# Kernel optimization log

Hardware: AMD Instinct MI355X
Metric: run time of the kernel (lower is better)

## Reference

```python
import jax, jax.numpy as jnp
import numpy as np

B, S, D, T = 512, 65536, 256, 10   # graphs, substructures, emb_dim, num_tasks
THRESHOLD = 0.4                    # CausalGNN threshold default
MEMBER_P = 0.002                   # ~131 substructures per graph


def setup_inputs() -> dict:
    key = jax.random.key(0)
    ks = jax.random.split(key, 8)
    def w(k, shape):
        fan_in = shape[0]
        return jax.random.normal(k, shape, jnp.float32) / np.float32(np.sqrt(fan_in))
    return {
        "h_graph": jax.random.normal(ks[0], (B, D), jnp.float32),
        "h_sub":   jax.random.normal(ks[1], (S, D), jnp.float32),
        "W1": w(ks[2], (D, 2 * D)),  "b1": jnp.zeros((2 * D,), jnp.float32),
        "W2": w(ks[3], (2 * D, 1)),  "b2": jnp.zeros((1,), jnp.float32),
        "Wc": w(ks[4], (2 * D, T)),  "bc": jnp.zeros((T,), jnp.float32),
        # dense [B,S] bool membership: mask[i,j] = substructure j belongs to graph i
        "mask": jax.random.bernoulli(ks[5], MEMBER_P, (B, S)),
    }


def _l2_normalize(x, eps=1e-12):  # F.normalize(p=2, dim=1)
    n = jnp.linalg.norm(x, axis=1, keepdims=True)
    return x / jnp.maximum(n, eps)


def reference(h_graph, h_sub, W1, b1, W2, b2, Wc, bc, mask):
    # SubMaskGenerator: Linear -> ReLU -> Dropout(eval=identity) -> Linear -> sigmoid, squeeze
    gate_logits = (jax.nn.relu(h_sub @ W1 + b1) @ W2 + b2)[:, 0]      # [S]
    subgraph_mask = jax.nn.sigmoid(gate_logits)                        # [S]

    # fused masked segment mean (replaces per-graph python loop + host sync):
    # valid[i,j] = (sub j in graph i) & (gate > threshold)
    valid = mask & (subgraph_mask > THRESHOLD)                         # [B,S] bool
    w = valid.astype(h_sub.dtype)
    counts = w.sum(axis=1, keepdims=True)                              # [B,1]
    sums = w @ h_sub                                                   # [B,D]
    h_sub_aligned = jnp.where(counts > 0, sums / jnp.maximum(counts, 1.0), 0.0)

    h_sub_norm = _l2_normalize(h_sub_aligned)
    h_graph_norm = _l2_normalize(h_graph)
    # F.cosine_similarity(dim=1, eps=1e-8) on the already-normalized vectors
    na = jnp.linalg.norm(h_sub_norm, axis=1)
    ng = jnp.linalg.norm(h_graph_norm, axis=1)
    cos = (h_sub_norm * h_graph_norm).sum(axis=1) / (
        jnp.maximum(na, 1e-8) * jnp.maximum(ng, 1e-8))
    cosine_loss = 1.0 - cos.mean()

    h_combined = jnp.concatenate([h_graph, h_sub_aligned], axis=1)     # [B,2D]
    logits = h_combined @ Wc + bc                                      # [B,T]
    return logits, cosine_loss, subgraph_mask
```

## Files before the change

kernel.cpp:

```cpp
#include <hip/hip_runtime.h>
#include <math.h>

#define D 256
#define H 512
#define TT 10
#define THRESH 0.4f
#define KS 8
#define NSPLIT 16

typedef __attribute__((ext_vector_type(8))) _Float16 half8;
typedef __attribute__((ext_vector_type(4))) float f32x4;

__global__ __launch_bounds__(256) void w1_prep(const float* __restrict__ W1,
                                               short* __restrict__ W1s)
{
    const int tid = blockIdx.x * 256 + threadIdx.x;
    const int lane = tid & 63;
    const int cell = tid >> 6;
    const int k = cell & 7;
    const int n = cell >> 3;
    const int row0 = k * 32 + (lane >> 4) * 8;
    const int col = n * 16 + (lane & 15);
    _Float16 h8[8];
    #pragma unroll
    for (int i = 0; i < 8; ++i)
        h8[i] = (_Float16)W1[(size_t)(row0 + i) * H + col];
    *reinterpret_cast<half8*>(W1s + (((size_t)n * 8 + k) * 64 + lane) * 8) =
        *reinterpret_cast<half8*>(h8);
}

__global__ __launch_bounds__(256, 2) void gate_mfma(
    const float* __restrict__ h_sub,
    const short* __restrict__ W1s,
    const float* __restrict__ b1,
    const float* __restrict__ W2,
    const float* __restrict__ b2,
    float* __restrict__ submask,
    unsigned* __restrict__ gbits)
{
    __shared__ __align__(16) short sB[2][16384];
    __shared__ float sb1[H], sw2[H];
    const int tid = threadIdx.x;
    const int lane = tid & 63;
    const int w = tid >> 6;
    const int base = blockIdx.x * 128 + w * 32;
    const int rot = blockIdx.x & 7;
    const float bb = b2[0];

    {
        int i = tid * 2;
        *reinterpret_cast<float2*>(&sb1[i]) = *reinterpret_cast<const float2*>(&b1[i]);
        *reinterpret_cast<float2*>(&sw2[i]) = *reinterpret_cast<const float2*>(&W2[i]);
    }

    half8 af[2][KS];
    #pragma unroll
    for (int s = 0; s < 2; ++s) {
        const int row = base + s * 16 + (lane & 15);
        const float* rp = h_sub + (size_t)row * D + (lane >> 4) * 8;
        #pragma unroll
        for (int k = 0; k < KS; ++k) {
            float x[8];
            *reinterpret_cast<float4*>(&x[0]) =
                *reinterpret_cast<const float4*>(rp + k * 32);
            *reinterpret_cast<float4*>(&x[4]) =
                *reinterpret_cast<const float4*>(rp + k * 32 + 4);
            _Float16 h8[8];
            #pragma unroll
            for (int i = 0; i < 8; ++i) h8[i] = (_Float16)x[i];
            af[s][k] = *reinterpret_cast<half8*>(h8);
        }
    }

    __syncthreads();

    auto stage = [&](int cc, int b) {
        const int c = (cc + rot) & 7;
        const char* gp = (const char*)W1s + ((size_t)c << 15) + (size_t)tid * 16;
        char* lp0 = (char*)&sB[b][0] + (size_t)tid * 16;
        #pragma unroll
        for (int i = 0; i < 8; ++i) {
            __builtin_amdgcn_global_load_lds(
                (const __attribute__((address_space(1))) void*)(gp + i * 4096),
                (__attribute__((address_space(3))) void*)(lp0 + i * 4096),
                16, 0, 0);
        }
    };

    stage(0, 0);
    stage(1, 1);

    float lp[2][4] = {{0.f,0.f,0.f,0.f},{0.f,0.f,0.f,0.f}};

    for (int cc = 0; cc < 8; ++cc) {
        if (cc < 7) asm volatile("s_waitcnt vmcnt(8)" ::: "memory");
        else        asm volatile("s_waitcnt vmcnt(0)" ::: "memory");
        __builtin_amdgcn_s_barrier();
        __builtin_amdgcn_sched_barrier(0);

        const short* buf = &sB[cc & 1][0];
        const int c = (cc + rot) & 7;

        f32x4 acc[2][4];
        #pragma unroll
        for (int s = 0; s < 2; ++s)
            #pragma unroll
            for (int nt = 0; nt < 4; ++nt)
                acc[s][nt] = (f32x4){0.f,0.f,0.f,0.f};

        __builtin_amdgcn_s_setprio(1);
        #pragma unroll
        for (int k = 0; k < KS; ++k) {
            half8 bh0 = *reinterpret_cast<const half8*>(buf + ((0 * 8 + k) * 64 + lane) * 8);
            half8 bh1 = *reinterpret_cast<const half8*>(buf + ((1 * 8 + k) * 64 + lane) * 8);
            half8 bh2 = *reinterpret_cast<const half8*>(buf + ((2 * 8 + k) * 64 + lane) * 8);
            half8 bh3 = *reinterpret_cast<const half8*>(buf + ((3 * 8 + k) * 64 + lane) * 8);
            acc[0][0] = __builtin_amdgcn_mfma_f32_16x16x32_f16(af[0][k], bh0, acc[0][0], 0, 0, 0);
            acc[1][0] = __builtin_amdgcn_mfma_f32_16x16x32_f16(af[1][k], bh0, acc[1][0], 0, 0, 0);
            acc[0][1] = __builtin_amdgcn_mfma_f32_16x16x32_f16(af[0][k], bh1, acc[0][1], 0, 0, 0);
            acc[1][1] = __builtin_amdgcn_mfma_f32_16x16x32_f16(af[1][k], bh1, acc[1][1], 0, 0, 0);
            acc[0][2] = __builtin_amdgcn_mfma_f32_16x16x32_f16(af[0][k], bh2, acc[0][2], 0, 0, 0);
            acc[1][2] = __builtin_amdgcn_mfma_f32_16x16x32_f16(af[1][k], bh2, acc[1][2], 0, 0, 0);
            acc[0][3] = __builtin_amdgcn_mfma_f32_16x16x32_f16(af[0][k], bh3, acc[0][3], 0, 0, 0);
            acc[1][3] = __builtin_amdgcn_mfma_f32_16x16x32_f16(af[1][k], bh3, acc[1][3], 0, 0, 0);
        }
        __builtin_amdgcn_s_setprio(0);

        #pragma unroll
        for (int nt = 0; nt < 4; ++nt) {
            const int hc = c * 64 + nt * 16 + (lane & 15);
            const float b1h = sb1[hc], w2h = sw2[hc];
            #pragma unroll
            for (int s = 0; s < 2; ++s)
                #pragma unroll
                for (int j = 0; j < 4; ++j) {
                    float v = acc[s][nt][j] + b1h;
                    v = v > 0.f ? v : 0.f;
                    lp[s][j] = fmaf(v, w2h, lp[s][j]);
                }
        }

        __builtin_amdgcn_sched_barrier(0);
        __builtin_amdgcn_s_barrier();
        if (cc < 6) stage(cc + 2, cc & 1);
    }

    #pragma unroll
    for (int m = 1; m < 16; m <<= 1)
        #pragma unroll
        for (int s = 0; s < 2; ++s)
            #pragma unroll
            for (int j = 0; j < 4; ++j)
                lp[s][j] += __shfl_xor(lp[s][j], m);

    const int g = lane >> 4;
    unsigned bits = 0;
    float sig[2][4];
    #pragma unroll
    for (int s = 0; s < 2; ++s)
        #pragma unroll
        for (int j = 0; j < 4; ++j) {
            sig[s][j] = 1.f / (1.f + expf(-(lp[s][j] + bb)));
            if (sig[s][j] > THRESH) bits |= 1u << (s * 16 + g * 4 + j);
        }
    bits |= __shfl_xor(bits, 16);
    bits |= __shfl_xor(bits, 32);
    if (lane == 0) gbits[blockIdx.x * 4 + w] = bits;

    if ((lane & 15) == 0)
        #pragma unroll
        for (int s = 0; s < 2; ++s)
            #pragma unroll
            for (int j = 0; j < 4; ++j)
                submask[base + s * 16 + g * 4 + j] = sig[s][j];
}

__global__ __launch_bounds__(256) void seg_scan(
    const float* __restrict__ h_sub,
    const int*   __restrict__ mask,
    const unsigned* __restrict__ gbits,
    float* __restrict__ psum,
    int*   __restrict__ pcnt,
    int S)
{
    const int i = blockIdx.x / NSPLIT;
    const int p = blockIdx.x % NSPLIT;
    const int tid = threadIdx.x;
    const int lane = tid & 63;
    const int w = tid >> 6;
    const int seg = S / NSPLIT;
    const int start = p * seg;
    const int* mrow = mask + (size_t)i * S + start;

    __shared__ unsigned sbits[4096 / 32];
    if (tid < seg / 32) sbits[tid] = gbits[(start >> 5) + tid];

    const int wbase = w * 1024;
    int4 m4[4];
    #pragma unroll
    for (int it = 0; it < 4; ++it)
        m4[it] = *reinterpret_cast<const int4*>(mrow + wbase + it * 256 + (lane << 2));

    __syncthreads();

    float4 acc = make_float4(0.f, 0.f, 0.f, 0.f);
    int cnt = 0;

    #pragma unroll
    for (int it = 0; it < 4; ++it) {
        const int j0 = wbase + it * 256 + (lane << 2);
        const unsigned bw = sbits[j0 >> 5];
        const int sh = j0 & 31;
        unsigned long long bal[4];
        bal[0] = __ballot((m4[it].x != 0) & ((bw >> (sh + 0)) & 1u));
        bal[1] = __ballot((m4[it].y != 0) & ((bw >> (sh + 1)) & 1u));
        bal[2] = __ballot((m4[it].z != 0) & ((bw >> (sh + 2)) & 1u));
        bal[3] = __ballot((m4[it].w != 0) & ((bw >> (sh + 3)) & 1u));
        #pragma unroll
        for (int s = 0; s < 4; ++s) {
            unsigned long long b = bal[s];
            while (b) {
                int t = __builtin_ctzll(b);
                b &= b - 1;
                int jj = start + wbase + it * 256 + (t << 2) + s;
                float4 hv = *reinterpret_cast<const float4*>(
                    h_sub + (size_t)jj * D + (lane << 2));
                acc.x += hv.x; acc.y += hv.y; acc.z += hv.z; acc.w += hv.w;
                cnt++;
            }
        }
    }

    __shared__ float ssum[4][D];
    __shared__ int   scnt[4];
    *reinterpret_cast<float4*>(&ssum[w][lane << 2]) = acc;
    if (lane == 0) scnt[w] = cnt;
    __syncthreads();

    float a = ssum[0][tid] + ssum[1][tid] + ssum[2][tid] + ssum[3][tid];
    psum[(size_t)blockIdx.x * D + tid] = a;
    if (tid == 0) pcnt[blockIdx.x] = scnt[0] + scnt[1] + scnt[2] + scnt[3];
}

__global__ __launch_bounds__(256) void seg_combine(
    const float* __restrict__ h_graph,
    const float* __restrict__ psum,
    const int*   __restrict__ pcnt,
    const float* __restrict__ Wc,
    const float* __restrict__ bc,
    float* __restrict__ logits,
    float* __restrict__ cos_ws)
{
    const int i = blockIdx.x;
    const int tid = threadIdx.x;
    const int lane = tid & 63;
    const int w = tid >> 6;

    float a = 0.f;
    int c = 0;
    #pragma unroll
    for (int p = 0; p < NSPLIT; ++p) {
        a += psum[((size_t)i * NSPLIT + p) * D + tid];
        c += pcnt[i * NSPLIT + p];
    }
    a = (c > 0) ? (a / (float)c) : 0.f;
    const float g = h_graph[(size_t)i * D + tid];

    float r0 = a * a, r1 = g * g, r2 = a * g;
    #pragma unroll
    for (int m = 1; m < 64; m <<= 1) {
        r0 += __shfl_xor(r0, m);
        r1 += __shfl_xor(r1, m);
        r2 += __shfl_xor(r2, m);
    }
    __shared__ float red[4][3];
    if (lane == 0) { red[w][0] = r0; red[w][1] = r1; red[w][2] = r2; }
    __syncthreads();
    if (tid == 0) {
        float a2 = red[0][0] + red[1][0] + red[2][0] + red[3][0];
        float g2 = red[0][1] + red[1][1] + red[2][1] + red[3][1];
        float ag = red[0][2] + red[1][2] + red[2][2] + red[3][2];
        float an = sqrtf(a2), gn = sqrtf(g2);
        float cs = (c > 0) ? (ag / (fmaxf(an, 1e-12f) * fmaxf(gn, 1e-12f))) : 0.f;
        cos_ws[i] = cs;
    }

    float lg[TT];
    #pragma unroll
    for (int t = 0; t < TT; ++t)
        lg[t] = g * Wc[(size_t)tid * TT + t] + a * Wc[(size_t)(D + tid) * TT + t];
    #pragma unroll
    for (int m = 1; m < 64; m <<= 1)
        #pragma unroll
        for (int t = 0; t < TT; ++t) lg[t] += __shfl_xor(lg[t], m);
    __shared__ float lpart[4][TT];
    if (lane == 0)
        #pragma unroll
        for (int t = 0; t < TT; ++t) lpart[w][t] = lg[t];
    __syncthreads();
    if (tid < TT)
        logits[(size_t)i * TT + tid] =
            lpart[0][tid] + lpart[1][tid] + lpart[2][tid] + lpart[3][tid] + bc[tid];
}

__global__ void loss_kernel(const float* __restrict__ cos_ws,
                            float* __restrict__ out, int B)
{
    const int lane = threadIdx.x;
    float s = 0.f;
    for (int i = lane; i < B; i += 64) s += cos_ws[i];
    #pragma unroll
    for (int m = 1; m < 64; m <<= 1) s += __shfl_xor(s, m);
    if (lane == 0) out[0] = 1.0f - s / (float)B;
}

extern "C" void kernel_launch(void* const* d_in, const int* in_sizes, int n_in,
                              void* d_out, int out_size, void* d_ws, size_t ws_size,
                              hipStream_t stream)
{
    const float* h_graph = (const float*)d_in[0];
    const float* h_sub   = (const float*)d_in[1];
    const float* W1      = (const float*)d_in[2];
    const float* b1      = (const float*)d_in[3];
    const float* W2      = (const float*)d_in[4];
    const float* b2      = (const float*)d_in[5];
    const float* Wc      = (const float*)d_in[6];
    const float* bc      = (const float*)d_in[7];
    const int*   mask    = (const int*)d_in[8];

    const int B = in_sizes[0] / D;
    const int S = in_sizes[1] / D;

    float* out     = (float*)d_out;
    float* logits  = out;
    float* loss    = out + (size_t)B * TT;
    float* submask = loss + 1;

    char* ws = (char*)d_ws;
    short*    W1s    = (short*)ws;
    unsigned* gbits  = (unsigned*)(ws + 512 * 1024);
    int*      pcnt   = (int*)(ws + 528 * 1024);
    float*    cos_ws = (float*)(ws + 576 * 1024);
    float*    psum   = (float*)(ws + 1024 * 1024);

    w1_prep<<<64, 256, 0, stream>>>(W1, W1s);
    gate_mfma<<<S / 128, 256, 0, stream>>>(h_sub, W1s, b1, W2, b2, submask, gbits);
    seg_scan<<<B * NSPLIT, 256, 0, stream>>>(h_sub, mask, gbits, psum, pcnt, S);
    seg_combine<<<B, 256, 0, stream>>>(h_graph, psum, pcnt, Wc, bc, logits, cos_ws);
    loss_kernel<<<1, 64, 0, stream>>>(cos_ws, loss, B);
}
```

Baseline: 71.66 us.

## Compress membership mask into bitmasks inside gate kernel with extra waves

The gate kernel grows to 512 threads: four waves keep doing the MFMA gate MLP while four new waves read the dense int32 membership mask and pack it into 64-bit ballot bitmasks in workspace. The seg_scan kernel then reads these compact bitmasks instead of the 128 MB int mask. The aim is to overlap the memory-bound mask read with the compute-bound gate work and shrink what seg_scan has to load. In exchange, the larger block may lower occupancy for the gate waves, and the mask waves have to join the gate waves' barriers.

```diff
diff --git a/kernel.cpp b/kernel.cpp
--- a/kernel.cpp
+++ b/kernel.cpp
@@ -29,50 +29,26 @@
         *reinterpret_cast<half8*>(h8);
 }
 
-__global__ __launch_bounds__(256, 2) void gate_mfma(
+__global__ __launch_bounds__(512, 4) void gate_fused(
     const float* __restrict__ h_sub,
     const short* __restrict__ W1s,
     const float* __restrict__ b1,
     const float* __restrict__ W2,
     const float* __restrict__ b2,
+    const int*   __restrict__ mask,
     float* __restrict__ submask,
-    unsigned* __restrict__ gbits)
+    unsigned* __restrict__ gbits,
+    unsigned long long* __restrict__ cmask)
 {
     __shared__ __align__(16) short sB[2][16384];
     __shared__ float sb1[H], sw2[H];
     const int tid = threadIdx.x;
     const int lane = tid & 63;
     const int w = tid >> 6;
+    const bool isGate = (w < 4);
     const int base = blockIdx.x * 128 + w * 32;
     const int rot = blockIdx.x & 7;
     const float bb = b2[0];
-
-    {
-        int i = tid * 2;
-        *reinterpret_cast<float2*>(&sb1[i]) = *reinterpret_cast<const float2*>(&b1[i]);
-        *reinterpret_cast<float2*>(&sw2[i]) = *reinterpret_cast<const float2*>(&W2[i]);
-    }
-
-    half8 af[2][KS];
-    #pragma unroll
-    for (int s = 0; s < 2; ++s) {
-        const int row = base + s * 16 + (lane & 15);
-        const float* rp = h_sub + (size_t)row * D + (lane >> 4) * 8;
-        #pragma unroll
-        for (int k = 0; k < KS; ++k) {
-            float x[8];
-            *reinterpret_cast<float4*>(&x[0]) =
-                *reinterpret_cast<const float4*>(rp + k * 32);
-            *reinterpret_cast<float4*>(&x[4]) =
-                *reinterpret_cast<const float4*>(rp + k * 32 + 4);
-            _Float16 h8[8];
-            #pragma unroll
-            for (int i = 0; i < 8; ++i) h8[i] = (_Float16)x[i];
-            af[s][k] = *reinterpret_cast<half8*>(h8);
-        }
-    }
-
-    __syncthreads();
 
     auto stage = [&](int cc, int b) {
         const int c = (cc + rot) & 7;
@@ -87,97 +63,152 @@
         }
     };
 
-    stage(0, 0);
-    stage(1, 1);
+    half8 af[2][KS];
+
+    if (isGate) {
+        stage(0, 0);
+        stage(1, 1);
+        int i = tid * 2;
+        *reinterpret_cast<float2*>(&sb1[i]) = *reinterpret_cast<const float2*>(&b1[i]);
+        *reinterpret_cast<float2*>(&sw2[i]) = *reinterpret_cast<const float2*>(&W2[i]);
+
+        #pragma unroll
+        for (int s = 0; s < 2; ++s) {
+            const int row = base + s * 16 + (lane & 15);
+            const float* rp = h_sub + (size_t)row * D + (lane >> 4) * 8;
+            #pragma unroll
+            for (int k = 0; k < KS; ++k) {
+                float x[8];
+                *reinterpret_cast<float4*>(&x[0]) =
+                    *reinterpret_cast<const float4*>(rp + k * 32);
+                *reinterpret_cast<float4*>(&x[4]) =
+                    *reinterpret_cast<const float4*>(rp + k * 32 + 4);
+                _Float16 h8[8];
+                #pragma unroll
+                for (int i2 = 0; i2 < 8; ++i2) h8[i2] = (_Float16)x[i2];
+                af[s][k] = *reinterpret_cast<half8*>(h8);
+            }
+        }
+    }
+
+    __syncthreads();
 
     float lp[2][4] = {{0.f,0.f,0.f,0.f},{0.f,0.f,0.f,0.f}};
+    const int mw = blockIdx.x * 4 + (w - 4);
+    const size_t g0 = (size_t)mw * 64;
 
     for (int cc = 0; cc < 8; ++cc) {
-        if (cc < 7) asm volatile("s_waitcnt vmcnt(8)" ::: "memory");
-        else        asm volatile("s_waitcnt vmcnt(0)" ::: "memory");
-        __builtin_amdgcn_s_barrier();
-        __builtin_amdgcn_sched_barrier(0);
-
-        const short* buf = &sB[cc & 1][0];
-        const int c = (cc + rot) & 7;
-
-        f32x4 acc[2][4];
+        if (isGate) {
+            if (cc < 7) asm volatile("s_waitcnt vmcnt(8)" ::: "memory");
+            else        asm volatile("s_waitcnt vmcnt(0)" ::: "memory");
+            __builtin_amdgcn_s_barrier();
+            __builtin_amdgcn_sched_barrier(0);
+
+            const short* buf = &sB[cc & 1][0];
+            const int c = (cc + rot) & 7;
+
+            f32x4 acc[2][4];
+            #pragma unroll
+            for (int s = 0; s < 2; ++s)
+                #pragma unroll
+                for (int nt = 0; nt < 4; ++nt)
+                    acc[s][nt] = (f32x4){0.f,0.f,0.f,0.f};
+
+            __builtin_amdgcn_s_setprio(1);
+            #pragma unroll
+            for (int k = 0; k < KS; ++k) {
+                half8 bh0 = *reinterpret_cast<const half8*>(buf + ((0 * 8 + k) * 64 + lane) * 8);
+                half8 bh1 = *reinterpret_cast<const half8*>(buf + ((1 * 8 + k) * 64 + lane) * 8);
+                half8 bh2 = *reinterpret_cast<const half8*>(buf + ((2 * 8 + k) * 64 + lane) * 8);
+                half8 bh3 = *reinterpret_cast<const half8*>(buf + ((3 * 8 + k) * 64 + lane) * 8);
+                acc[0][0] = __builtin_amdgcn_mfma_f32_16x16x32_f16(af[0][k], bh0, acc[0][0], 0, 0, 0);
+                acc[1][0] = __builtin_amdgcn_mfma_f32_16x16x32_f16(af[1][k], bh0, acc[1][0], 0, 0, 0);
+                acc[0][1] = __builtin_amdgcn_mfma_f32_16x16x32_f16(af[0][k], bh1, acc[0][1], 0, 0, 0);
+                acc[1][1] = __builtin_amdgcn_mfma_f32_16x16x32_f16(af[1][k], bh1, acc[1][1], 0, 0, 0);
+                acc[0][2] = __builtin_amdgcn_mfma_f32_16x16x32_f16(af[0][k], bh2, acc[0][2], 0, 0, 0);
+                acc[1][2] = __builtin_amdgcn_mfma_f32_16x16x32_f16(af[1][k], bh2, acc[1][2], 0, 0, 0);
+                acc[0][3] = __builtin_amdgcn_mfma_f32_16x16x32_f16(af[0][k], bh3, acc[0][3], 0, 0, 0);
+                acc[1][3] = __builtin_amdgcn_mfma_f32_16x16x32_f16(af[1][k], bh3, acc[1][3], 0, 0, 0);
+            }
+            __builtin_amdgcn_s_setprio(0);
+
+            #pragma unroll
+            for (int nt = 0; nt < 4; ++nt) {
+                const int hc = c * 64 + nt * 16 + (lane & 15);
+                const float b1h = sb1[hc], w2h = sw2[hc];
+                #pragma unroll
+                for (int s = 0; s < 2; ++s)
+                    #pragma unroll
+                    for (int j = 0; j < 4; ++j) {
+                        float v = acc[s][nt][j] + b1h;
+                        v = v > 0.f ? v : 0.f;
+                        lp[s][j] = fmaf(v, w2h, lp[s][j]);
+                    }
+            }
+
+            __builtin_amdgcn_sched_barrier(0);
+            __builtin_amdgcn_s_barrier();
+            if (cc < 6) stage(cc + 2, cc & 1);
+        } else {
+            __builtin_amdgcn_s_barrier();
+            {
+                const size_t gbase = g0 + (size_t)cc * 8;
+                int4 m4[8];
+                #pragma unroll
+                for (int u = 0; u < 8; ++u)
+                    m4[u] = *reinterpret_cast<const int4*>(
+                        mask + (gbase + u) * 256 + (lane << 2));
+                #pragma unroll
+                for (int u = 0; u < 8; ++u) {
+                    unsigned long long c0 = __ballot(m4[u].x != 0);
+                    unsigned long long c1 = __ballot(m4[u].y != 0);
+                    unsigned long long c2 = __ballot(m4[u].z != 0);
+                    unsigned long long c3 = __ballot(m4[u].w != 0);
+                    if (lane == 0) {
+                        unsigned long long* cp = cmask + (gbase + u) * 4;
+                        cp[0] = c0; cp[1] = c1; cp[2] = c2; cp[3] = c3;
+                    }
+                }
+            }
+            __builtin_amdgcn_s_barrier();
+        }
+    }
+
+    if (isGate) {
+        #pragma unroll
+        for (int m = 1; m < 16; m <<= 1)
+            #pragma unroll
+            for (int s = 0; s < 2; ++s)
+                #pragma unroll
+                for (int j = 0; j < 4; ++j)
+                    lp[s][j] += __shfl_xor(lp[s][j], m);
+
+        const int g = lane >> 4;
+        unsigned bits = 0;
+        float sig[2][4];
         #pragma unroll
         for (int s = 0; s < 2; ++s)
             #pragma unroll
-            for (int nt = 0; nt < 4; ++nt)
-                acc[s][nt] = (f32x4){0.f,0.f,0.f,0.f};
-
-        __builtin_amdgcn_s_setprio(1);
-        #pragma unroll
-        for (int k = 0; k < KS; ++k) {
-            half8 bh0 = *reinterpret_cast<const half8*>(buf + ((0 * 8 + k) * 64 + lane) * 8);
-            half8 bh1 = *reinterpret_cast<const half8*>(buf + ((1 * 8 + k) * 64 + lane) * 8);
-            half8 bh2 = *reinterpret_cast<const half8*>(buf + ((2 * 8 + k) * 64 + lane) * 8);
-            half8 bh3 = *reinterpret_cast<const half8*>(buf + ((3 * 8 + k) * 64 + lane) * 8);
-            acc[0][0] = __builtin_amdgcn_mfma_f32_16x16x32_f16(af[0][k], bh0, acc[0][0], 0, 0, 0);
-            acc[1][0] = __builtin_amdgcn_mfma_f32_16x16x32_f16(af[1][k], bh0, acc[1][0], 0, 0, 0);
-            acc[0][1] = __builtin_amdgcn_mfma_f32_16x16x32_f16(af[0][k], bh1, acc[0][1], 0, 0, 0);
-            acc[1][1] = __builtin_amdgcn_mfma_f32_16x16x32_f16(af[1][k], bh1, acc[1][1], 0, 0, 0);
-            acc[0][2] = __builtin_amdgcn_mfma_f32_16x16x32_f16(af[0][k], bh2, acc[0][2], 0, 0, 0);
-            acc[1][2] = __builtin_amdgcn_mfma_f32_16x16x32_f16(af[1][k], bh2, acc[1][2], 0, 0, 0);
-            acc[0][3] = __builtin_amdgcn_mfma_f32_16x16x32_f16(af[0][k], bh3, acc[0][3], 0, 0, 0);
-            acc[1][3] = __builtin_amdgcn_mfma_f32_16x16x32_f16(af[1][k], bh3, acc[1][3], 0, 0, 0);
-        }
-        __builtin_amdgcn_s_setprio(0);
-
-        #pragma unroll
-        for (int nt = 0; nt < 4; ++nt) {
-            const int hc = c * 64 + nt * 16 + (lane & 15);
-            const float b1h = sb1[hc], w2h = sw2[hc];
+            for (int j = 0; j < 4; ++j) {
+                sig[s][j] = 1.f / (1.f + expf(-(lp[s][j] + bb)));
+                if (sig[s][j] > THRESH) bits |= 1u << (s * 16 + g * 4 + j);
+            }
+        bits |= __shfl_xor(bits, 16);
+        bits |= __shfl_xor(bits, 32);
+        if (lane == 0) gbits[blockIdx.x * 4 + w] = bits;
+
+        if ((lane & 15) == 0)
             #pragma unroll
             for (int s = 0; s < 2; ++s)
                 #pragma unroll
-                for (int j = 0; j < 4; ++j) {
-                    float v = acc[s][nt][j] + b1h;
-                    v = v > 0.f ? v : 0.f;
-                    lp[s][j] = fmaf(v, w2h, lp[s][j]);
-                }
-        }
-
-        __builtin_amdgcn_sched_barrier(0);
-        __builtin_amdgcn_s_barrier();
-        if (cc < 6) stage(cc + 2, cc & 1);
-    }
-
-    #pragma unroll
-    for (int m = 1; m < 16; m <<= 1)
-        #pragma unroll
-        for (int s = 0; s < 2; ++s)
-            #pragma unroll
-            for (int j = 0; j < 4; ++j)
-                lp[s][j] += __shfl_xor(lp[s][j], m);
-
-    const int g = lane >> 4;
-    unsigned bits = 0;
-    float sig[2][4];
-    #pragma unroll
-    for (int s = 0; s < 2; ++s)
-        #pragma unroll
-        for (int j = 0; j < 4; ++j) {
-            sig[s][j] = 1.f / (1.f + expf(-(lp[s][j] + bb)));
-            if (sig[s][j] > THRESH) bits |= 1u << (s * 16 + g * 4 + j);
-        }
-    bits |= __shfl_xor(bits, 16);
-    bits |= __shfl_xor(bits, 32);
-    if (lane == 0) gbits[blockIdx.x * 4 + w] = bits;
-
-    if ((lane & 15) == 0)
-        #pragma unroll
-        for (int s = 0; s < 2; ++s)
-            #pragma unroll
-            for (int j = 0; j < 4; ++j)
-                submask[base + s * 16 + g * 4 + j] = sig[s][j];
+                for (int j = 0; j < 4; ++j)
+                    submask[base + s * 16 + g * 4 + j] = sig[s][j];
+    }
 }
 
 __global__ __launch_bounds__(256) void seg_scan(
     const float* __restrict__ h_sub,
-    const int*   __restrict__ mask,
+    const unsigned long long* __restrict__ cmask,
     const unsigned* __restrict__ gbits,
     float* __restrict__ psum,
     int*   __restrict__ pcnt,
@@ -190,17 +221,11 @@
     const int w = tid >> 6;
     const int seg = S / NSPLIT;
     const int start = p * seg;
-    const int* mrow = mask + (size_t)i * S + start;
+    const unsigned long long* cm =
+        cmask + ((size_t)i * (S / 256) + (size_t)p * (seg / 256)) * 4;
 
     __shared__ unsigned sbits[4096 / 32];
     if (tid < seg / 32) sbits[tid] = gbits[(start >> 5) + tid];
-
-    const int wbase = w * 1024;
-    int4 m4[4];
-    #pragma unroll
-    for (int it = 0; it < 4; ++it)
-        m4[it] = *reinterpret_cast<const int4*>(mrow + wbase + it * 256 + (lane << 2));
-
     __syncthreads();
 
     float4 acc = make_float4(0.f, 0.f, 0.f, 0.f);
@@ -208,21 +233,22 @@
 
     #pragma unroll
     for (int it = 0; it < 4; ++it) {
-        const int j0 = wbase + it * 256 + (lane << 2);
+        const int g = w * 4 + it;
+        const int j0 = g * 256 + (lane << 2);
         const unsigned bw = sbits[j0 >> 5];
         const int sh = j0 & 31;
         unsigned long long bal[4];
-        bal[0] = __ballot((m4[it].x != 0) & ((bw >> (sh + 0)) & 1u));
-        bal[1] = __ballot((m4[it].y != 0) & ((bw >> (sh + 1)) & 1u));
-        bal[2] = __ballot((m4[it].z != 0) & ((bw >> (sh + 2)) & 1u));
-        bal[3] = __ballot((m4[it].w != 0) & ((bw >> (sh + 3)) & 1u));
+        bal[0] = __ballot((bw >> (sh + 0)) & 1u) & cm[(size_t)g * 4 + 0];
+        bal[1] = __ballot((bw >> (sh + 1)) & 1u) & cm[(size_t)g * 4 + 1];
+        bal[2] = __ballot((bw >> (sh + 2)) & 1u) & cm[(size_t)g * 4 + 2];
+        bal[3] = __ballot((bw >> (sh + 3)) & 1u) & cm[(size_t)g * 4 + 3];
         #pragma unroll
         for (int s = 0; s < 4; ++s) {
             unsigned long long b = bal[s];
             while (b) {
                 int t = __builtin_ctzll(b);
                 b &= b - 1;
-                int jj = start + wbase + it * 256 + (t << 2) + s;
+                int jj = start + g * 256 + (t << 2) + s;
                 float4 hv = *reinterpret_cast<const float4*>(
                     h_sub + (size_t)jj * D + (lane << 2));
                 acc.x += hv.x; acc.y += hv.y; acc.z += hv.z; acc.w += hv.w;
@@ -342,10 +368,13 @@
     int*      pcnt   = (int*)(ws + 528 * 1024);
     float*    cos_ws = (float*)(ws + 576 * 1024);
     float*    psum   = (float*)(ws + 1024 * 1024);
+    unsigned long long* cmask =
+        (unsigned long long*)(ws + 16 * 1024 * 1024);
 
     w1_prep<<<64, 256, 0, stream>>>(W1, W1s);
-    gate_mfma<<<S / 128, 256, 0, stream>>>(h_sub, W1s, b1, W2, b2, submask, gbits);
-    seg_scan<<<B * NSPLIT, 256, 0, stream>>>(h_sub, mask, gbits, psum, pcnt, S);
+    gate_fused<<<S / 128, 512, 0, stream>>>(
+        h_sub, W1s, b1, W2, b2, mask, submask, gbits, cmask);
+    seg_scan<<<B * NSPLIT, 256, 0, stream>>>(h_sub, cmask, gbits, psum, pcnt, S);
     seg_combine<<<B, 256, 0, stream>>>(h_graph, psum, pcnt, Wc, bc, logits, cos_ws);
     loss_kernel<<<1, 64, 0, stream>>>(cos_ws, loss, B);
 }
```

Result: slower. 73.42 us (+2.5%).
